# Optimization experiments

Measured on AMD Instinct MI355X. Metric: run time of the kernel, lower is better.

Reference implementation:

```python
import jax, jax.numpy as jnp
import numpy as np

NF = 64      # num_feat
NFR = 5      # num_frames
G = 8        # offset/deformable groups
CENTER = NFR // 2
K = 9        # 3x3 taps


def conv3x3(x, w, b):
    y = jax.lax.conv_general_dilated(x, w, (1, 1), 'SAME',
                                     dimension_numbers=('NCHW', 'OIHW', 'NCHW'))
    return y + b[None, :, None, None]


def mdcn(x, offsets, masks, w, b):
    # x: [B,C,H,W]; offsets: [B,2*G*K,H,W] (layout g,k,(y,x)); masks: [B,G*K,H,W]
    B, C, H, W = x.shape
    Cg = C // G
    off = offsets.reshape(B, G, K, 2, H, W)
    oy, ox = off[:, :, :, 0], off[:, :, :, 1]          # [B,G,K,H,W]
    m = masks.reshape(B, G, K, H, W)
    ky = jnp.repeat(jnp.arange(3), 3) - 1              # [K]
    kx = jnp.tile(jnp.arange(3), 3) - 1
    base_y = (ky[:, None, None] + jnp.arange(H)[None, :, None]).astype(x.dtype)  # [K,H,1]
    base_x = (kx[:, None, None] + jnp.arange(W)[None, None, :]).astype(x.dtype)  # [K,1,W]
    py = oy + base_y[None, None]                        # [B,G,K,H,W]
    px = ox + base_x[None, None]
    y0f = jnp.floor(py); x0f = jnp.floor(px)
    ty = py - y0f; tx = px - x0f
    y0 = y0f.astype(jnp.int32); x0 = x0f.astype(jnp.int32)
    xg = x.reshape(B, G, Cg, H * W)

    def gather(yi, xi):
        valid = (yi >= 0) & (yi < H) & (xi >= 0) & (xi < W)
        yc = jnp.clip(yi, 0, H - 1); xc = jnp.clip(xi, 0, W - 1)
        idx = (yc * W + xc).reshape(B, G, 1, K * H * W)
        idx = jnp.broadcast_to(idx, (B, G, Cg, K * H * W))
        v = jnp.take_along_axis(xg, idx, axis=3).reshape(B, G, Cg, K, H, W)
        return v * valid.reshape(B, G, 1, K, H, W)

    v00 = gather(y0, x0); v01 = gather(y0, x0 + 1)
    v10 = gather(y0 + 1, x0); v11 = gather(y0 + 1, x0 + 1)
    ty_ = ty[:, :, None]; tx_ = tx[:, :, None]          # [B,G,1,K,H,W]
    samp = (v00 * (1 - ty_) * (1 - tx_) + v01 * (1 - ty_) * tx_ +
            v10 * ty_ * (1 - tx_) + v11 * ty_ * tx_)
    samp = samp * m[:, :, None]                          # modulation
    wr = w.reshape(-1, G, Cg, K)                         # [Cout,G,Cg,K]
    out = jnp.einsum('bgckhw,ogck->bohw', samp, wr)
    return out + b[None, :, None, None]


def setup_inputs():
    key = jax.random.key(0)
    ks = jax.random.split(key, 16)
    def mk(k, shape, fan_in):
        return jax.random.normal(k, shape, jnp.float32) * (1.0 / np.sqrt(fan_in))
    B, H, W = 1, 160, 160
    return {
        'x':   jax.random.normal(ks[0], (B, NFR, 4, H, W), jnp.float32),
        'fw1': mk(ks[1], (NF, 4, 3, 3), 4 * 9),   'fb1': jnp.zeros((NF,), jnp.float32),
        'fw2': mk(ks[2], (NF, NF, 3, 3), NF * 9), 'fb2': jnp.zeros((NF,), jnp.float32),
        'fw3': mk(ks[3], (NF, NF, 3, 3), NF * 9), 'fb3': jnp.zeros((NF,), jnp.float32),
        'ow1': mk(ks[4], (NF, 2 * NF, 3, 3), 2 * NF * 9), 'ob1': jnp.zeros((NF,), jnp.float32),
        'ow2': mk(ks[5], (NF, NF, 3, 3), NF * 9),         'ob2': jnp.zeros((NF,), jnp.float32),
        'ow3': mk(ks[6], (G * 27, NF, 3, 3), NF * 9) * 0.1,
        'ob3': jnp.zeros((G * 27,), jnp.float32),
        'dw':  mk(ks[7], (NF, NF, 3, 3), NF * 9), 'db': jnp.zeros((NF,), jnp.float32),
    }


def reference(x, fw1, fb1, fw2, fb2, fw3, fb3, ow1, ob1, ow2, ob2, ow3, ob3, dw, db):
    B, N, C, H, W = x.shape
    f = x.reshape(B * N, C, H, W)
    f = jax.nn.relu(conv3x3(f, fw1, fb1))
    f = jax.nn.relu(conv3x3(f, fw2, fb2))
    f = jax.nn.relu(conv3x3(f, fw3, fb3))
    feats = f.reshape(B, N, NF, H, W)
    ref = feats[:, CENTER]                               # [B,NF,H,W]
    nc = np.array([i for i in range(N) if i != CENTER])
    curr = feats[:, nc].reshape(B * (N - 1), NF, H, W)
    ref_t = jnp.broadcast_to(ref[:, None], (B, N - 1, NF, H, W)).reshape(B * (N - 1), NF, H, W)
    cat = jnp.concatenate([ref_t, curr], axis=1)         # [B(N-1),2*NF,H,W]
    o = jax.nn.relu(conv3x3(cat, ow1, ob1))
    o = jax.nn.relu(conv3x3(o, ow2, ob2))
    raw = conv3x3(o, ow3, ob3)                           # [B(N-1),27G,H,W]
    offsets = raw[:, :G * 18]
    masks = jax.nn.sigmoid(raw[:, G * 18:])
    aligned = mdcn(curr, offsets, masks, dw, db)
    aligned = aligned.reshape(B, N - 1, NF, H, W)
    return jnp.concatenate([aligned[:, :CENTER], ref[:, None], aligned[:, CENTER:]], axis=1)
```

## Files before the change

### kernel.cpp

```cpp
#include <hip/hip_runtime.h>
#include <hip/hip_bf16.h>
#include <math.h>

#define HH 160
#define WW 160
#define HWsz (HH*WW)

typedef short bf16x8 __attribute__((ext_vector_type(8)));
typedef float f32x4  __attribute__((ext_vector_type(4)));

__device__ inline ushort f2bf(float f) {
    unsigned int u = __float_as_uint(f);
    unsigned int r = (u + 0x7FFFu + ((u >> 16) & 1u)) >> 16;
    return (ushort)r;
}

__device__ inline void unpk8(uint4 u, float* f) {
    f[0] = __uint_as_float(u.x << 16); f[1] = __uint_as_float(u.x & 0xFFFF0000u);
    f[2] = __uint_as_float(u.y << 16); f[3] = __uint_as_float(u.y & 0xFFFF0000u);
    f[4] = __uint_as_float(u.z << 16); f[5] = __uint_as_float(u.z & 0xFFFF0000u);
    f[6] = __uint_as_float(u.w << 16); f[7] = __uint_as_float(u.w & 0xFFFF0000u);
}

__global__ __launch_bounds__(256)
void pack_all(const float* __restrict__ fw2, const float* __restrict__ fw3,
              const float* __restrict__ ow1, const float* __restrict__ ow2,
              const float* __restrict__ ow3, const float* __restrict__ dw,
              ushort* __restrict__ w2p, ushort* __restrict__ w3p,
              ushort* __restrict__ o1p, ushort* __restrict__ o2p,
              ushort* __restrict__ o3p, ushort* __restrict__ wmp)
{
    const int seg = blockIdx.y;
    const int idx = blockIdx.x * 256 + threadIdx.x;

    if (seg == 5) {
        if (idx >= 18 * 4 * 64) return;
        const int lane = idx & 63;
        const int mt   = (idx >> 6) & 3;
        const int chunk = idx >> 8;
        const int o  = mt * 16 + (lane & 15);
        const int gk = chunk * 4 + (lane >> 4);
        const int g  = gk / 9, k = gk % 9;
        ushort v[8];
#pragma unroll
        for (int j = 0; j < 8; ++j)
            v[j] = f2bf(dw[((size_t)o * 64 + g * 8 + j) * 9 + k]);
        uint4 pk;
        pk.x = (unsigned)v[0] | ((unsigned)v[1] << 16);
        pk.y = (unsigned)v[2] | ((unsigned)v[3] << 16);
        pk.z = (unsigned)v[4] | ((unsigned)v[5] << 16);
        pk.w = (unsigned)v[6] | ((unsigned)v[7] << 16);
        *(uint4*)(wmp + (size_t)idx * 8) = pk;
        return;
    }

    const float* w; ushort* wp; int Cout, Cin, MT_TOT, CIC;
    switch (seg) {
        case 0: w = fw2; wp = w2p; Cout = 64;  Cin = 64;  MT_TOT = 4;  CIC = 2; break;
        case 1: w = fw3; wp = w3p; Cout = 64;  Cin = 64;  MT_TOT = 4;  CIC = 2; break;
        case 2: w = ow1; wp = o1p; Cout = 64;  Cin = 128; MT_TOT = 4;  CIC = 4; break;
        case 3: w = ow2; wp = o2p; Cout = 64;  Cin = 64;  MT_TOT = 4;  CIC = 2; break;
        default: w = ow3; wp = o3p; Cout = 216; Cin = 64; MT_TOT = 16; CIC = 2; break;
    }
    const int total = 9 * CIC * MT_TOT * 64;
    if (idx >= total) return;
    const int lane = idx & 63;
    int t = idx >> 6;
    const int mt  = t % MT_TOT; t /= MT_TOT;
    const int cic = t % CIC;    t /= CIC;
    const int tap = t;
    const int co  = mt * 16 + (lane & 15);
    const int ci0 = cic * 32 + (lane >> 4) * 8;
    ushort v[8];
#pragma unroll
    for (int j = 0; j < 8; ++j) {
        const int ci = ci0 + j;
        float f = 0.f;
        if (co < Cout && ci < Cin) f = w[((size_t)co * Cin + ci) * 9 + tap];
        v[j] = f2bf(f);
    }
    uint4 pk;
    pk.x = (unsigned)v[0] | ((unsigned)v[1] << 16);
    pk.y = (unsigned)v[2] | ((unsigned)v[3] << 16);
    pk.z = (unsigned)v[4] | ((unsigned)v[5] << 16);
    pk.w = (unsigned)v[6] | ((unsigned)v[7] << 16);
    *(uint4*)(wp + (size_t)idx * 8) = pk;
}

template<int CI_STEPS, bool CONCAT, bool RELU, int OMODE>
__global__ __launch_bounds__(256, 2)
void mfma_conv(const ushort* __restrict__ in, const ushort* __restrict__ wp,
               const float* __restrict__ bias, void* __restrict__ outv,
               int Cout, int MT_TOT, int COG,
               float* __restrict__ outmain, ushort* __restrict__ aux)
{
    constexpr int ROWS = 8, HR = ROWS + 2, NT = 4;
    constexpr int C8   = 8;
    constexpr int CICT = 2 * CI_STEPS;
    constexpr int CIN  = CICT * 32;
    __shared__ uint4 s_in4[HR * 34 * C8];
    __shared__ uint4 s_a4[9 * 4 * 64];

    const int tid = threadIdx.x;
    const int lane = tid & 63, wid = tid >> 6;
    const int lane15 = lane & 15, lgrp = lane >> 4;
    const int bz = blockIdx.z;
    const int frame = bz / COG, cog = bz % COG;
    const int x0 = blockIdx.x * 32, y0 = blockIdx.y * ROWS;

    const ushort* src = nullptr; const ushort* srcRef = nullptr; const ushort* srcCur = nullptr;
    if (CONCAT) {
        const int fidx = (frame < 2) ? frame : frame + 1;
        srcRef = in + (size_t)2 * HWsz * 64;
        srcCur = in + (size_t)fidx * HWsz * 64;
    } else {
        src = in + (size_t)frame * HWsz * CIN;
    }

    f32x4 acc[4][NT];
#pragma unroll
    for (int m = 0; m < 4; ++m)
#pragma unroll
        for (int n = 0; n < NT; ++n) acc[m][n] = (f32x4){0.f, 0.f, 0.f, 0.f};

    const uint4* wp4 = (const uint4*)wp;
    const int wrow = wid * 2;
    const int mtg0 = cog * 4;

#pragma unroll
    for (int step = 0; step < CI_STEPS; ++step) {
#pragma unroll
        for (int half = 0; half < 2; ++half) {
            if (half == 0) {
                for (int i = tid; i < HR * 34 * C8; i += 256) {
                    const int ci8l = i & (C8 - 1);
                    const int rem = i / C8;
                    const int col = rem % 34, row = rem / 34;
                    const int gy = y0 + row - 1, gx = x0 + col - 1;
                    const int gci8 = step * C8 + ci8l;
                    uint4 v = {0u, 0u, 0u, 0u};
                    if (gy >= 0 && gy < HH && gx >= 0 && gx < WW) {
                        if (CONCAT) {
                            const ushort* sp = (gci8 < 8) ? srcRef : srcCur;
                            v = *(const uint4*)(sp + (size_t)(gy * WW + gx) * 64 + (gci8 & 7) * 8);
                        } else {
                            v = *(const uint4*)(src + (size_t)(gy * WW + gx) * CIN + gci8 * 8);
                        }
                    }
                    s_in4[(row * 34 + col) * C8 + (ci8l ^ (col & 7))] = v;
                }
            }
#pragma unroll
            for (int it = 0; it < 9; ++it) {
                const int i = tid + it * 256;
                const int ln = i & 63, mt = (i >> 6) & 3, kkl = i >> 8;
                const int kkg = half * 9 + kkl;
                const int tap = kkg >> 1, cic = kkg & 1;
                s_a4[i] = wp4[((size_t)(tap * CICT + step * 2 + cic) * MT_TOT + mtg0 + mt) * 64 + ln];
            }
            __syncthreads();

#pragma unroll
            for (int kkl = 0; kkl < 9; ++kkl) {
                const int kkg = half * 9 + kkl;
                const int tap = kkg >> 1, cic = kkg & 1;
                const int dy  = tap / 3 - 1;
                const int dxp = tap % 3;
                bf16x8 a[4];
#pragma unroll
                for (int mt = 0; mt < 4; ++mt)
                    a[mt] = *(const bf16x8*)&s_a4[(kkl * 4 + mt) * 64 + lane];
#pragma unroll
                for (int nt = 0; nt < NT; ++nt) {
                    const int row_l = wrow + (nt >> 1) + dy + 1;
                    const int col_l = (nt & 1) * 16 + lane15 + dxp;
                    const bf16x8 b = *(const bf16x8*)
                        &s_in4[(row_l * 34 + col_l) * C8 + ((cic * 4 + lgrp) ^ (col_l & 7))];
#pragma unroll
                    for (int mt = 0; mt < 4; ++mt)
                        acc[mt][nt] = __builtin_amdgcn_mfma_f32_16x16x32_bf16(a[mt], b, acc[mt][nt], 0, 0, 0);
                }
            }
            __syncthreads();
        }
    }

#pragma unroll
    for (int mt = 0; mt < 4; ++mt) {
        const int co = cog * 64 + mt * 16 + lgrp * 4;
        if (co < Cout) {
            const float4 bs = *(const float4*)&bias[co];
#pragma unroll
            for (int nt = 0; nt < NT; ++nt) {
                const int yy = y0 + wrow + (nt >> 1);
                const int xx = x0 + (nt & 1) * 16 + lane15;
                const int hw = yy * WW + xx;
                f32x4 v = acc[mt][nt];
                v[0] += bs.x; v[1] += bs.y; v[2] += bs.z; v[3] += bs.w;
                if (RELU) {
                    v[0] = fmaxf(v[0], 0.f); v[1] = fmaxf(v[1], 0.f);
                    v[2] = fmaxf(v[2], 0.f); v[3] = fmaxf(v[3], 0.f);
                }
                if (OMODE <= 1) {
                    uint2 pk;
                    pk.x = (unsigned)f2bf(v[0]) | ((unsigned)f2bf(v[1]) << 16);
                    pk.y = (unsigned)f2bf(v[2]) | ((unsigned)f2bf(v[3]) << 16);
                    *(uint2*)((ushort*)outv + ((size_t)frame * HWsz + hw) * 64 + co) = pk;
                    if (OMODE == 1) {
                        if (frame == 2) {
#pragma unroll
                            for (int j = 0; j < 4; ++j)
                                outmain[((size_t)(128 + co + j)) * HWsz + hw] = v[j];
                        } else {
                            const int b = (frame < 2) ? frame : frame - 1;
                            *(uint2*)(aux + (((size_t)(b * 8 + (co >> 3)) * HWsz + hw) * 8 + (co & 7))) = pk;
                        }
                    }
                } else {
                    const ushort h0 = f2bf(v[0]), h1 = f2bf(v[1]);
                    const ushort h2 = f2bf(v[2]), h3 = f2bf(v[3]);
                    if (co < 144) {
                        unsigned* roff = (unsigned*)outv + (size_t)frame * 72 * HWsz;
                        roff[(size_t)(co >> 1) * HWsz + hw]       = (unsigned)h0 | ((unsigned)h1 << 16);
                        roff[(size_t)((co >> 1) + 1) * HWsz + hw] = (unsigned)h2 | ((unsigned)h3 << 16);
                    } else {
                        ushort* rmsk = aux + (size_t)frame * 72 * HWsz;
                        const int gk0 = co - 144;
                        rmsk[(size_t)(gk0 + 0) * HWsz + hw] = h0;
                        rmsk[(size_t)(gk0 + 1) * HWsz + hw] = h1;
                        rmsk[(size_t)(gk0 + 2) * HWsz + hw] = h2;
                        rmsk[(size_t)(gk0 + 3) * HWsz + hw] = h3;
                    }
                }
            }
        }
    }
}

__global__ __launch_bounds__(256)
void conv1_kernel(const float* __restrict__ x, const float* __restrict__ w,
                  const float* __restrict__ b, ushort* __restrict__ out)
{
    const int fr = blockIdx.z;
    const int t = threadIdx.x;
    const int tx = t & 15, ty = t >> 4;
    const int x0 = blockIdx.x * 16, y0 = blockIdx.y * 16;

    __shared__ float s_x[4][18][18];
    __shared__ float s_w[36][64];
    __shared__ float s_b[64];

    for (int i = t; i < 4 * 18 * 18; i += 256) {
        const int ci = i / 324, rem = i % 324;
        const int yy = rem / 18, xx = rem % 18;
        const int gy = y0 + yy - 1, gx = x0 + xx - 1;
        float v = 0.f;
        if (gy >= 0 && gy < HH && gx >= 0 && gx < WW)
            v = x[((size_t)fr * 4 + ci) * HWsz + gy * WW + gx];
        s_x[ci][yy][xx] = v;
    }
    for (int i = t; i < 36 * 64; i += 256) {
        const int row = i / 64, o = i % 64;
        const int ci = row / 9, tap = row % 9;
        s_w[row][o] = w[((size_t)o * 4 + ci) * 9 + tap];
    }
    if (t < 64) s_b[t] = b[t];
    __syncthreads();

    float acc[64];
#pragma unroll
    for (int i = 0; i < 64; ++i) acc[i] = 0.f;

#pragma unroll
    for (int ci = 0; ci < 4; ++ci) {
#pragma unroll
        for (int tap = 0; tap < 9; ++tap) {
            const float v = s_x[ci][ty + tap / 3][tx + tap % 3];
            const float4* wr = (const float4*)&s_w[ci * 9 + tap][0];
#pragma unroll
            for (int o4 = 0; o4 < 16; ++o4) {
                const float4 wv = wr[o4];
                acc[o4 * 4 + 0] = fmaf(v, wv.x, acc[o4 * 4 + 0]);
                acc[o4 * 4 + 1] = fmaf(v, wv.y, acc[o4 * 4 + 1]);
                acc[o4 * 4 + 2] = fmaf(v, wv.z, acc[o4 * 4 + 2]);
                acc[o4 * 4 + 3] = fmaf(v, wv.w, acc[o4 * 4 + 3]);
            }
        }
    }

    ushort* ob = out + ((size_t)fr * HWsz + (y0 + ty) * WW + (x0 + tx)) * 64;
#pragma unroll
    for (int o8 = 0; o8 < 8; ++o8) {
        ushort v[8];
#pragma unroll
        for (int j = 0; j < 8; ++j)
            v[j] = f2bf(fmaxf(acc[o8 * 8 + j] + s_b[o8 * 8 + j], 0.f));
        uint4 pk;
        pk.x = (unsigned)v[0] | ((unsigned)v[1] << 16);
        pk.y = (unsigned)v[2] | ((unsigned)v[3] << 16);
        pk.z = (unsigned)v[4] | ((unsigned)v[5] << 16);
        pk.w = (unsigned)v[6] | ((unsigned)v[7] << 16);
        *(uint4*)(ob + o8 * 8) = pk;
    }
}

__global__ __launch_bounds__(256)
void mdcn_mfma(const ushort* __restrict__ ftsg, const unsigned* __restrict__ roffg,
               const ushort* __restrict__ rmskg,
               const ushort* __restrict__ wmp, const float* __restrict__ db,
               float* __restrict__ out)
{
    const int b    = blockIdx.z;
    const int fidx = (b < 2) ? b : b + 1;
    const int tid  = threadIdx.x;
    const int lane = tid & 63, wid = tid >> 6;
    const int lane15 = lane & 15, lgrp = lane >> 4;
    const int x = blockIdx.x * 16 + lane15;
    const int y = blockIdx.y * 4 + wid;
    const int hw = y * WW + x;

    const unsigned* roff = roffg + (size_t)b * 72 * HWsz;
    const ushort*   rmsk = rmskg + (size_t)b * 72 * HWsz;
    const uint4* wmp4 = (const uint4*)wmp;

    f32x4 acc[4];
#pragma unroll
    for (int m = 0; m < 4; ++m) acc[m] = (f32x4){0.f, 0.f, 0.f, 0.f};

#pragma unroll 2
    for (int chunk = 0; chunk < 18; ++chunk) {
        const int gk = chunk * 4 + lgrp;
        const int g  = gk / 9, k = gk - 9 * g;
        const int kyy = k / 3 - 1, kxx = k % 3 - 1;

        const unsigned op = roff[(size_t)gk * HWsz + hw];
        const ushort   mu = rmsk[(size_t)gk * HWsz + hw];
        const float oy = __uint_as_float(op << 16);
        const float ox = __uint_as_float(op & 0xFFFF0000u);
        const float mraw = __uint_as_float((unsigned)mu << 16);
        const float mv = 1.f / (1.f + __expf(-mraw));

        const float py = oy + (float)(y + kyy);
        const float px = ox + (float)(x + kxx);
        const float y0f = floorf(py), x0f = floorf(px);
        const float tyf = py - y0f, txf = px - x0f;
        const int y0 = (int)y0f, x0i = (int)x0f;
        const int y1 = y0 + 1, x1 = x0i + 1;
        const bool vy0 = (y0 >= 0) & (y0 < HH);
        const bool vy1 = (y1 >= 0) & (y1 < HH);
        const bool vx0 = (x0i >= 0) & (x0i < WW);
        const bool vx1 = (x1 >= 0) & (x1 < WW);
        const int yc0 = min(max(y0, 0), HH - 1), yc1 = min(max(y1, 0), HH - 1);
        const int xc0 = min(max(x0i, 0), WW - 1), xc1 = min(max(x1, 0), WW - 1);
        const float a0 = (1.f - tyf) * mv, a1 = tyf * mv;
        float w00 = a0 * (1.f - txf);
        float w01 = a0 * txf;
        float w10 = a1 * (1.f - txf);
        float w11 = a1 * txf;
        if (!(vy0 && vx0)) w00 = 0.f;
        if (!(vy0 && vx1)) w01 = 0.f;
        if (!(vy1 && vx0)) w10 = 0.f;
        if (!(vy1 && vx1)) w11 = 0.f;

        const ushort* pb = ftsg + (size_t)(b * 8 + g) * HWsz * 8;
        const uint4 u00 = *(const uint4*)(pb + (size_t)(yc0 * WW + xc0) * 8);
        const uint4 u01 = *(const uint4*)(pb + (size_t)(yc0 * WW + xc1) * 8);
        const uint4 u10 = *(const uint4*)(pb + (size_t)(yc1 * WW + xc0) * 8);
        const uint4 u11 = *(const uint4*)(pb + (size_t)(yc1 * WW + xc1) * 8);
        float f00[8], f01[8], f10[8], f11[8];
        unpk8(u00, f00); unpk8(u01, f01); unpk8(u10, f10); unpk8(u11, f11);

        float s[8];
#pragma unroll
        for (int c = 0; c < 8; ++c)
            s[c] = fmaf(w11, f11[c], fmaf(w10, f10[c],
                    fmaf(w01, f01[c], w00 * f00[c])));
        uint4 bpk;
        asm("v_cvt_pk_bf16_f32 %0, %1, %2" : "=v"(bpk.x) : "v"(s[0]), "v"(s[1]));
        asm("v_cvt_pk_bf16_f32 %0, %1, %2" : "=v"(bpk.y) : "v"(s[2]), "v"(s[3]));
        asm("v_cvt_pk_bf16_f32 %0, %1, %2" : "=v"(bpk.z) : "v"(s[4]), "v"(s[5]));
        asm("v_cvt_pk_bf16_f32 %0, %1, %2" : "=v"(bpk.w) : "v"(s[6]), "v"(s[7]));
        const bf16x8 bfrag = __builtin_bit_cast(bf16x8, bpk);

#pragma unroll
        for (int mt = 0; mt < 4; ++mt) {
            const bf16x8 a = *(const bf16x8*)&wmp4[(size_t)(chunk * 4 + mt) * 64 + lane];
            acc[mt] = __builtin_amdgcn_mfma_f32_16x16x32_bf16(a, bfrag, acc[mt], 0, 0, 0);
        }
    }

    float* ob = out + (size_t)fidx * 64 * HWsz + hw;
#pragma unroll
    for (int mt = 0; mt < 4; ++mt) {
        const int o0 = mt * 16 + lgrp * 4;
        const float4 bs = *(const float4*)&db[o0];
        ob[(size_t)(o0 + 0) * HWsz] = acc[mt][0] + bs.x;
        ob[(size_t)(o0 + 1) * HWsz] = acc[mt][1] + bs.y;
        ob[(size_t)(o0 + 2) * HWsz] = acc[mt][2] + bs.z;
        ob[(size_t)(o0 + 3) * HWsz] = acc[mt][3] + bs.w;
    }
}

extern "C" void kernel_launch(void* const* d_in, const int* in_sizes, int n_in,
                              void* d_out, int out_size, void* d_ws, size_t ws_size,
                              hipStream_t stream)
{
    const float* x   = (const float*)d_in[0];
    const float* fw1 = (const float*)d_in[1];
    const float* fb1 = (const float*)d_in[2];
    const float* fw2 = (const float*)d_in[3];
    const float* fb2 = (const float*)d_in[4];
    const float* fw3 = (const float*)d_in[5];
    const float* fb3 = (const float*)d_in[6];
    const float* ow1 = (const float*)d_in[7];
    const float* ob1 = (const float*)d_in[8];
    const float* ow2 = (const float*)d_in[9];
    const float* ob2 = (const float*)d_in[10];
    const float* ow3 = (const float*)d_in[11];
    const float* ob3 = (const float*)d_in[12];
    const float* dw  = (const float*)d_in[13];
    const float* db  = (const float*)d_in[14];
    float* out = (float*)d_out;

    ushort* buf1 = (ushort*)d_ws;
    ushort* buf2 = buf1 + (size_t)5 * HWsz * 64;
    ushort* fts  = buf2 + (size_t)5 * HWsz * 64;
    ushort* ftsg = fts + (size_t)5 * HWsz * 64;
    unsigned* roff = (unsigned*)(ftsg + (size_t)4 * 8 * HWsz * 8);
    ushort* rmsk = (ushort*)(roff + (size_t)4 * 72 * HWsz);
    ushort* w2p  = rmsk + (size_t)4 * 72 * HWsz;
    ushort* w3p  = w2p + 36864;
    ushort* o1p  = w3p + 36864;
    ushort* o2p  = o1p + 73728;
    ushort* o3p  = o2p + 36864;
    ushort* wmp  = o3p + 147456;

    const dim3 blk(256);

    pack_all<<<dim3(72, 6), blk, 0, stream>>>(fw2, fw3, ow1, ow2, ow3, dw,
                                              w2p, w3p, o1p, o2p, o3p, wmp);

    conv1_kernel<<<dim3(10, 10, 5), blk, 0, stream>>>(x, fw1, fb1, buf1);
    mfma_conv<1, false, true, 0><<<dim3(5, 20, 5), blk, 0, stream>>>(
        buf1, w2p, fb2, buf2, 64, 4, 1, nullptr, nullptr);
    mfma_conv<1, false, true, 1><<<dim3(5, 20, 5), blk, 0, stream>>>(
        buf2, w3p, fb3, fts, 64, 4, 1, out, ftsg);

    mfma_conv<2, true, true, 0><<<dim3(5, 20, 4), blk, 0, stream>>>(
        fts, o1p, ob1, buf1, 64, 4, 1, nullptr, nullptr);
    mfma_conv<1, false, true, 0><<<dim3(5, 20, 4), blk, 0, stream>>>(
        buf1, o2p, ob2, buf2, 64, 4, 1, nullptr, nullptr);
    mfma_conv<1, false, false, 3><<<dim3(5, 20, 16), blk, 0, stream>>>(
        buf2, o3p, ob3, roff, 216, 16, 4, nullptr, rmsk);

    mdcn_mfma<<<dim3(10, 40, 4), blk, 0, stream>>>(ftsg, roff, rmsk, wmp, db, out);
}
```

Measured before the change: 197.8 us.

## Stream conv weights via double buffer, move sigmoid upstream, software-pipeline MDCN gathers

The conv kernel now streams weight tiles through a two-slot shared buffer with register prefetch instead of staging nine taps per half, which cuts shared memory so occupancy can be raised to 3 blocks. That adds a barrier after every tap. The mask sigmoid moves from the deformable kernel into the offset-conv epilogue. The deformable kernel uses 512-thread blocks, caches the modulation weights in shared memory, preloads offsets into registers, and software-pipelines the bilinear gathers one group ahead. This costs extra registers.

```diff
diff --git a/kernel.cpp b/kernel.cpp
--- a/kernel.cpp
+++ b/kernel.cpp
@@ -88,7 +88,7 @@
 }
 
 template<int CI_STEPS, bool CONCAT, bool RELU, int OMODE>
-__global__ __launch_bounds__(256, 2)
+__global__ __launch_bounds__(256, 3)
 void mfma_conv(const ushort* __restrict__ in, const ushort* __restrict__ wp,
                const float* __restrict__ bias, void* __restrict__ outv,
                int Cout, int MT_TOT, int COG,
@@ -99,7 +99,7 @@
     constexpr int CICT = 2 * CI_STEPS;
     constexpr int CIN  = CICT * 32;
     __shared__ uint4 s_in4[HR * 34 * C8];
-    __shared__ uint4 s_a4[9 * 4 * 64];
+    __shared__ uint4 s_a4[2][256];
 
     const int tid = threadIdx.x;
     const int lane = tid & 63, wid = tid >> 6;
@@ -126,61 +126,56 @@
     const uint4* wp4 = (const uint4*)wp;
     const int wrow = wid * 2;
     const int mtg0 = cog * 4;
+    const int amt = tid >> 6, aln = tid & 63;
 
 #pragma unroll
     for (int step = 0; step < CI_STEPS; ++step) {
-#pragma unroll
-        for (int half = 0; half < 2; ++half) {
-            if (half == 0) {
-                for (int i = tid; i < HR * 34 * C8; i += 256) {
-                    const int ci8l = i & (C8 - 1);
-                    const int rem = i / C8;
-                    const int col = rem % 34, row = rem / 34;
-                    const int gy = y0 + row - 1, gx = x0 + col - 1;
-                    const int gci8 = step * C8 + ci8l;
-                    uint4 v = {0u, 0u, 0u, 0u};
-                    if (gy >= 0 && gy < HH && gx >= 0 && gx < WW) {
-                        if (CONCAT) {
-                            const ushort* sp = (gci8 < 8) ? srcRef : srcCur;
-                            v = *(const uint4*)(sp + (size_t)(gy * WW + gx) * 64 + (gci8 & 7) * 8);
-                        } else {
-                            v = *(const uint4*)(src + (size_t)(gy * WW + gx) * CIN + gci8 * 8);
-                        }
-                    }
-                    s_in4[(row * 34 + col) * C8 + (ci8l ^ (col & 7))] = v;
+        uint4 areg = wp4[((size_t)(0 * CICT + step * 2 + 0) * MT_TOT + mtg0 + amt) * 64 + aln];
+        for (int i = tid; i < HR * 34 * C8; i += 256) {
+            const int ci8l = i & (C8 - 1);
+            const int rem = i / C8;
+            const int col = rem % 34, row = rem / 34;
+            const int gy = y0 + row - 1, gx = x0 + col - 1;
+            const int gci8 = step * C8 + ci8l;
+            uint4 v = {0u, 0u, 0u, 0u};
+            if (gy >= 0 && gy < HH && gx >= 0 && gx < WW) {
+                if (CONCAT) {
+                    const ushort* sp = (gci8 < 8) ? srcRef : srcCur;
+                    v = *(const uint4*)(sp + (size_t)(gy * WW + gx) * 64 + (gci8 & 7) * 8);
+                } else {
+                    v = *(const uint4*)(src + (size_t)(gy * WW + gx) * CIN + gci8 * 8);
                 }
             }
-#pragma unroll
-            for (int it = 0; it < 9; ++it) {
-                const int i = tid + it * 256;
-                const int ln = i & 63, mt = (i >> 6) & 3, kkl = i >> 8;
-                const int kkg = half * 9 + kkl;
-                const int tap = kkg >> 1, cic = kkg & 1;
-                s_a4[i] = wp4[((size_t)(tap * CICT + step * 2 + cic) * MT_TOT + mtg0 + mt) * 64 + ln];
+            s_in4[(row * 34 + col) * C8 + (ci8l ^ (col & 7))] = v;
+        }
+        s_a4[0][tid] = areg;
+        __syncthreads();
+
+#pragma unroll
+        for (int kk = 0; kk < 18; ++kk) {
+            const int tap = kk >> 1, cic = kk & 1;
+            const int dy  = tap / 3 - 1;
+            const int dxp = tap % 3;
+            uint4 nreg;
+            if (kk < 17) {
+                const int ntap = (kk + 1) >> 1, ncic = (kk + 1) & 1;
+                nreg = wp4[((size_t)(ntap * CICT + step * 2 + ncic) * MT_TOT + mtg0 + amt) * 64 + aln];
             }
-            __syncthreads();
-
-#pragma unroll
-            for (int kkl = 0; kkl < 9; ++kkl) {
-                const int kkg = half * 9 + kkl;
-                const int tap = kkg >> 1, cic = kkg & 1;
-                const int dy  = tap / 3 - 1;
-                const int dxp = tap % 3;
-                bf16x8 a[4];
+            bf16x8 a[4];
+#pragma unroll
+            for (int mt = 0; mt < 4; ++mt)
+                a[mt] = *(const bf16x8*)&s_a4[kk & 1][mt * 64 + lane];
+#pragma unroll
+            for (int nt = 0; nt < NT; ++nt) {
+                const int row_l = wrow + (nt >> 1) + dy + 1;
+                const int col_l = (nt & 1) * 16 + lane15 + dxp;
+                const bf16x8 b = *(const bf16x8*)
+                    &s_in4[(row_l * 34 + col_l) * C8 + ((cic * 4 + lgrp) ^ (col_l & 7))];
 #pragma unroll
                 for (int mt = 0; mt < 4; ++mt)
-                    a[mt] = *(const bf16x8*)&s_a4[(kkl * 4 + mt) * 64 + lane];
-#pragma unroll
-                for (int nt = 0; nt < NT; ++nt) {
-                    const int row_l = wrow + (nt >> 1) + dy + 1;
-                    const int col_l = (nt & 1) * 16 + lane15 + dxp;
-                    const bf16x8 b = *(const bf16x8*)
-                        &s_in4[(row_l * 34 + col_l) * C8 + ((cic * 4 + lgrp) ^ (col_l & 7))];
-#pragma unroll
-                    for (int mt = 0; mt < 4; ++mt)
-                        acc[mt][nt] = __builtin_amdgcn_mfma_f32_16x16x32_bf16(a[mt], b, acc[mt][nt], 0, 0, 0);
-                }
+                    acc[mt][nt] = __builtin_amdgcn_mfma_f32_16x16x32_bf16(a[mt], b, acc[mt][nt], 0, 0, 0);
             }
+            if (kk < 17) s_a4[(kk + 1) & 1][tid] = nreg;
             __syncthreads();
         }
     }
@@ -217,19 +212,20 @@
                         }
                     }
                 } else {
-                    const ushort h0 = f2bf(v[0]), h1 = f2bf(v[1]);
-                    const ushort h2 = f2bf(v[2]), h3 = f2bf(v[3]);
                     if (co < 144) {
+                        const ushort h0 = f2bf(v[0]), h1 = f2bf(v[1]);
+                        const ushort h2 = f2bf(v[2]), h3 = f2bf(v[3]);
                         unsigned* roff = (unsigned*)outv + (size_t)frame * 72 * HWsz;
                         roff[(size_t)(co >> 1) * HWsz + hw]       = (unsigned)h0 | ((unsigned)h1 << 16);
                         roff[(size_t)((co >> 1) + 1) * HWsz + hw] = (unsigned)h2 | ((unsigned)h3 << 16);
                     } else {
                         ushort* rmsk = aux + (size_t)frame * 72 * HWsz;
                         const int gk0 = co - 144;
-                        rmsk[(size_t)(gk0 + 0) * HWsz + hw] = h0;
-                        rmsk[(size_t)(gk0 + 1) * HWsz + hw] = h1;
-                        rmsk[(size_t)(gk0 + 2) * HWsz + hw] = h2;
-                        rmsk[(size_t)(gk0 + 3) * HWsz + hw] = h3;
+#pragma unroll
+                        for (int j = 0; j < 4; ++j) {
+                            const float m = 1.f / (1.f + __expf(-v[j]));
+                            rmsk[(size_t)(gk0 + j) * HWsz + hw] = f2bf(m);
+                        }
                     }
                 }
             }
@@ -304,41 +300,49 @@
     }
 }
 
-__global__ __launch_bounds__(256)
+__global__ __launch_bounds__(512, 4)
 void mdcn_mfma(const ushort* __restrict__ ftsg, const unsigned* __restrict__ roffg,
                const ushort* __restrict__ rmskg,
                const ushort* __restrict__ wmp, const float* __restrict__ db,
                float* __restrict__ out)
 {
+    __shared__ uint4 s_w4[18 * 4 * 64];
+
     const int b    = blockIdx.z;
     const int fidx = (b < 2) ? b : b + 1;
     const int tid  = threadIdx.x;
     const int lane = tid & 63, wid = tid >> 6;
     const int lane15 = lane & 15, lgrp = lane >> 4;
     const int x = blockIdx.x * 16 + lane15;
-    const int y = blockIdx.y * 4 + wid;
+    const int y = blockIdx.y * 8 + wid;
     const int hw = y * WW + x;
+
+    const uint4* wmp4 = (const uint4*)wmp;
+    for (int i = tid; i < 18 * 4 * 64; i += 512) s_w4[i] = wmp4[i];
 
     const unsigned* roff = roffg + (size_t)b * 72 * HWsz;
     const ushort*   rmsk = rmskg + (size_t)b * 72 * HWsz;
-    const uint4* wmp4 = (const uint4*)wmp;
+
+    unsigned opv[18];
+#pragma unroll
+    for (int n = 0; n < 18; ++n)
+        opv[n] = roff[(size_t)(n * 4 + lgrp) * HWsz + hw];
+
+    __syncthreads();
 
     f32x4 acc[4];
 #pragma unroll
     for (int m = 0; m < 4; ++m) acc[m] = (f32x4){0.f, 0.f, 0.f, 0.f};
 
-#pragma unroll 2
-    for (int chunk = 0; chunk < 18; ++chunk) {
-        const int gk = chunk * 4 + lgrp;
-        const int g  = gk / 9, k = gk - 9 * g;
-        const int kyy = k / 3 - 1, kxx = k % 3 - 1;
-
-        const unsigned op = roff[(size_t)gk * HWsz + hw];
-        const ushort   mu = rmsk[(size_t)gk * HWsz + hw];
+    auto prep = [&](int n, uint4& u00, uint4& u01, uint4& u10, uint4& u11,
+                    float& w00, float& w01, float& w10, float& w11) {
+        const int gk = n * 4 + lgrp;
+        const int gg = gk / 9, k9 = gk - 9 * gg;
+        const int kyy = k9 / 3 - 1, kxx = k9 - (k9 / 3) * 3 - 1;
+        const unsigned op = opv[n];
         const float oy = __uint_as_float(op << 16);
         const float ox = __uint_as_float(op & 0xFFFF0000u);
-        const float mraw = __uint_as_float((unsigned)mu << 16);
-        const float mv = 1.f / (1.f + __expf(-mraw));
+        const float mv = __uint_as_float((unsigned)rmsk[(size_t)gk * HWsz + hw] << 16);
 
         const float py = oy + (float)(y + kyy);
         const float px = ox + (float)(x + kxx);
@@ -353,28 +357,40 @@
         const int yc0 = min(max(y0, 0), HH - 1), yc1 = min(max(y1, 0), HH - 1);
         const int xc0 = min(max(x0i, 0), WW - 1), xc1 = min(max(x1, 0), WW - 1);
         const float a0 = (1.f - tyf) * mv, a1 = tyf * mv;
-        float w00 = a0 * (1.f - txf);
-        float w01 = a0 * txf;
-        float w10 = a1 * (1.f - txf);
-        float w11 = a1 * txf;
+        w00 = a0 * (1.f - txf);
+        w01 = a0 * txf;
+        w10 = a1 * (1.f - txf);
+        w11 = a1 * txf;
         if (!(vy0 && vx0)) w00 = 0.f;
         if (!(vy0 && vx1)) w01 = 0.f;
         if (!(vy1 && vx0)) w10 = 0.f;
         if (!(vy1 && vx1)) w11 = 0.f;
 
-        const ushort* pb = ftsg + (size_t)(b * 8 + g) * HWsz * 8;
-        const uint4 u00 = *(const uint4*)(pb + (size_t)(yc0 * WW + xc0) * 8);
-        const uint4 u01 = *(const uint4*)(pb + (size_t)(yc0 * WW + xc1) * 8);
-        const uint4 u10 = *(const uint4*)(pb + (size_t)(yc1 * WW + xc0) * 8);
-        const uint4 u11 = *(const uint4*)(pb + (size_t)(yc1 * WW + xc1) * 8);
+        const ushort* pb = ftsg + (size_t)(b * 8 + gg) * HWsz * 8;
+        u00 = *(const uint4*)(pb + (size_t)(yc0 * WW + xc0) * 8);
+        u01 = *(const uint4*)(pb + (size_t)(yc0 * WW + xc1) * 8);
+        u10 = *(const uint4*)(pb + (size_t)(yc1 * WW + xc0) * 8);
+        u11 = *(const uint4*)(pb + (size_t)(yc1 * WW + xc1) * 8);
+    };
+
+    uint4 cu00, cu01, cu10, cu11;
+    float cw00, cw01, cw10, cw11;
+    prep(0, cu00, cu01, cu10, cu11, cw00, cw01, cw10, cw11);
+
+#pragma unroll
+    for (int g = 0; g < 18; ++g) {
+        uint4 nu00, nu01, nu10, nu11;
+        float nw00, nw01, nw10, nw11;
+        if (g < 17)
+            prep(g + 1, nu00, nu01, nu10, nu11, nw00, nw01, nw10, nw11);
+
         float f00[8], f01[8], f10[8], f11[8];
-        unpk8(u00, f00); unpk8(u01, f01); unpk8(u10, f10); unpk8(u11, f11);
-
+        unpk8(cu00, f00); unpk8(cu01, f01); unpk8(cu10, f10); unpk8(cu11, f11);
         float s[8];
 #pragma unroll
         for (int c = 0; c < 8; ++c)
-            s[c] = fmaf(w11, f11[c], fmaf(w10, f10[c],
-                    fmaf(w01, f01[c], w00 * f00[c])));
+            s[c] = fmaf(cw11, f11[c], fmaf(cw10, f10[c],
+                    fmaf(cw01, f01[c], cw00 * f00[c])));
         uint4 bpk;
         asm("v_cvt_pk_bf16_f32 %0, %1, %2" : "=v"(bpk.x) : "v"(s[0]), "v"(s[1]));
         asm("v_cvt_pk_bf16_f32 %0, %1, %2" : "=v"(bpk.y) : "v"(s[2]), "v"(s[3]));
@@ -384,8 +400,13 @@
 
 #pragma unroll
         for (int mt = 0; mt < 4; ++mt) {
-            const bf16x8 a = *(const bf16x8*)&wmp4[(size_t)(chunk * 4 + mt) * 64 + lane];
+            const bf16x8 a = *(const bf16x8*)&s_w4[(g * 4 + mt) * 64 + lane];
             acc[mt] = __builtin_amdgcn_mfma_f32_16x16x32_bf16(a, bfrag, acc[mt], 0, 0, 0);
+        }
+
+        if (g < 17) {
+            cu00 = nu00; cu01 = nu01; cu10 = nu10; cu11 = nu11;
+            cw00 = nw00; cw01 = nw01; cw10 = nw10; cw11 = nw11;
         }
     }
 
@@ -453,5 +474,5 @@
     mfma_conv<1, false, false, 3><<<dim3(5, 20, 16), blk, 0, stream>>>(
         buf2, o3p, ob3, roff, 216, 16, 4, nullptr, rmsk);
 
-    mdcn_mfma<<<dim3(10, 40, 4), blk, 0, stream>>>(ftsg, roff, rmsk, wmp, db, out);
-}
+    mdcn_mfma<<<dim3(10, 20, 4), dim3(512), 0, stream>>>(ftsg, roff, rmsk, wmp, db, out);
+}
```

Measured after the change: 222.9 us. +12.7%, slower.
